# Performance work log

Measured on AMD Instinct MI355X. Metric: run time of the kernel, lower is better.

The kernel has to match this reference:

```python
import jax, jax.numpy as jnp
import numpy as np

N, E, D_IN, H, C, N_GRAPHS = 50000, 800000, 128, 2, 64, 50
D_HID = H * C  # 128
NEG_SLOPE = 0.2
EPS = 1e-16


def glorot(key, shape):
    fan_in, fan_out = shape[0], shape[-1]
    lim = jnp.sqrt(6.0 / (fan_in + fan_out))
    return jax.random.uniform(key, shape, jnp.float32, -lim, lim)


def setup_inputs() -> dict:
    key = jax.random.key(0)
    ks = jax.random.split(key, 12)
    x = jax.random.normal(ks[0], (N, D_IN), jnp.float32)
    edge_index = jax.random.randint(ks[1], (2, E), 0, N, jnp.int64)
    batch = jnp.sort(jax.random.randint(ks[2], (N,), 0, N_GRAPHS, jnp.int64))
    # GATConv layer 1: in=128 -> heads=2, out=64
    W1 = glorot(ks[3], (D_IN, H * C))
    as1 = glorot(ks[4], (1, H, C)).reshape(H, C)
    ad1 = glorot(ks[5], (1, H, C)).reshape(H, C)
    b1 = jnp.zeros((H * C,), jnp.float32)
    # GATConv layer 2: in=128 -> heads=2, out=64
    W2 = glorot(ks[6], (D_HID, H * C))
    as2 = glorot(ks[7], (1, H, C)).reshape(H, C)
    ad2 = glorot(ks[8], (1, H, C)).reshape(H, C)
    b2 = jnp.zeros((H * C,), jnp.float32)
    # Linear head: 128 -> 1
    Wh = glorot(ks[9], (D_HID, 1))
    bh = jnp.zeros((1,), jnp.float32)
    return {"x": x, "edge_index": edge_index, "batch": batch,
            "W1": W1, "as1": as1, "ad1": ad1, "b1": b1,
            "W2": W2, "as2": as2, "ad2": ad2, "b2": b2,
            "Wh": Wh, "bh": bh}


def gat_conv(x, src, dst, W, a_src, a_dst, bias):
    # PyG GATConv (concat=True, add_self_loops applied by caller, eval mode)
    n = x.shape[0]
    h = (x @ W).reshape(n, H, C)                       # [N,H,C]
    al_s = jnp.einsum('nhc,hc->nh', h, a_src)          # [N,H]
    al_d = jnp.einsum('nhc,hc->nh', h, a_dst)
    e = jax.nn.leaky_relu(al_s[src] + al_d[dst], NEG_SLOPE)  # [E',H]
    # segment softmax over incoming edges of each dst node
    e_max = jax.ops.segment_max(e, dst, num_segments=n)
    e = jnp.exp(e - e_max[dst])
    denom = jax.ops.segment_sum(e, dst, num_segments=n)
    alpha = e / (denom[dst] + EPS)                     # [E',H]
    out = jax.ops.segment_sum(alpha[:, :, None] * h[src], dst, num_segments=n)
    return out.reshape(n, H * C) + bias


def reference(x, edge_index, batch, W1, as1, ad1, b1, W2, as2, ad2, b2, Wh, bh):
    # add self-loops (PyG GATConv default)
    loops = jnp.arange(N, dtype=edge_index.dtype)
    src = jnp.concatenate([edge_index[0], loops])
    dst = jnp.concatenate([edge_index[1], loops])
    h = gat_conv(x, src, dst, W1, as1, ad1, b1)
    h = jax.nn.relu(h)  # dropout is identity in eval mode
    h = gat_conv(h, src, dst, W2, as2, ad2, b2)
    h = jax.nn.relu(h)
    # global mean pool over graphs
    sums = jax.ops.segment_sum(h, batch, num_segments=N_GRAPHS)
    counts = jax.ops.segment_sum(jnp.ones((N, 1), h.dtype), batch, num_segments=N_GRAPHS)
    pooled = sums / jnp.maximum(counts, 1.0)           # [G, 128]
    return pooled @ Wh + bh                            # [G, 1]
```

## Files before the change

### kernel.cpp

```cpp
#include <hip/hip_runtime.h>
#include <hip/hip_fp16.h>
#include <math.h>

#define HD 128
#define NEG_SLOPE 0.2f
#define EPSV 1e-16f
#define TILE 8192

typedef unsigned short ushort_t;
typedef __attribute__((ext_vector_type(8))) short bf16x8;
typedef __attribute__((ext_vector_type(4))) float f32x4;

__device__ inline void bsplit(float x, ushort_t& hi, ushort_t& lo) {
    unsigned u = __float_as_uint(x);
    unsigned hb = (u + 0x7FFFu + ((u >> 16) & 1u)) >> 16;
    hi = (ushort_t)hb;
    float res = x - __uint_as_float(hb << 16);
    unsigned v = __float_as_uint(res);
    lo = (ushort_t)((v + 0x7FFFu + ((v >> 16) & 1u)) >> 16);
}

__global__ __launch_bounds__(256) void part_hist(const int* __restrict__ dst,
                                                 int* __restrict__ tileHist, int E) {
    __shared__ int hist[256];
    int t = threadIdx.x;
    hist[t] = 0;
    __syncthreads();
    int base = blockIdx.x * TILE;
    int end = base + TILE; if (end > E) end = E;
    for (int i = base + t; i < end; i += 256)
        atomicAdd(&hist[dst[i] >> 8], 1);
    __syncthreads();
    tileHist[blockIdx.x * 256 + t] = hist[t];
}

__global__ __launch_bounds__(256) void part_offsets(int* __restrict__ tileHist,
                                                    int* __restrict__ bucketBase,
                                                    int NT) {
    __shared__ int s[256];
    int b = threadIdx.x;
    int total = 0;
    #pragma unroll 8
    for (int t = 0; t < NT; ++t) total += tileHist[t * 256 + b];
    s[b] = total;
    __syncthreads();
    for (int o = 1; o < 256; o <<= 1) {
        int v = (b >= o) ? s[b - o] : 0;
        __syncthreads();
        s[b] += v;
        __syncthreads();
    }
    int base = (b == 0) ? 0 : s[b - 1];
    bucketBase[b] = base;
    if (b == 255) bucketBase[256] = s[255];
    int run = base;
    #pragma unroll 8
    for (int t = 0; t < NT; ++t) {
        int v = tileHist[t * 256 + b];
        tileHist[t * 256 + b] = run;
        run += v;
    }
}

__global__ __launch_bounds__(256) void part_scatter(const int* __restrict__ src,
                                                    const int* __restrict__ dst,
                                                    const int* __restrict__ tileHist,
                                                    int* __restrict__ part, int E) {
    __shared__ int cur[256];
    int t = threadIdx.x;
    cur[t] = tileHist[blockIdx.x * 256 + t];
    __syncthreads();
    int base = blockIdx.x * TILE;
    int end = base + TILE; if (end > E) end = E;
    for (int i = base + t; i < end; i += 256) {
        int d = dst[i], s = src[i];
        int p = atomicAdd(&cur[d >> 8], 1);
        part[p] = (s << 8) | (d & 255);
    }
}

__global__ __launch_bounds__(256) void fine_counts(const int* __restrict__ part,
                                                   const int* __restrict__ bucketBase,
                                                   int* __restrict__ cnt,
                                                   int* __restrict__ bsum, int N) {
    __shared__ int hist[256];
    int t = threadIdx.x;
    hist[t] = 0;
    __syncthreads();
    int b = blockIdx.x;
    int s0 = bucketBase[b], s1 = bucketBase[b + 1];
    for (int i = s0 + t; i < s1; i += 256)
        atomicAdd(&hist[part[i] & 255], 1);
    __syncthreads();
    int d = b * 256 + t;
    if (d < N) cnt[d] = hist[t] + 1;
    if (t == 0) {
        int nn = N - b * 256; if (nn > 256) nn = 256; if (nn < 0) nn = 0;
        bsum[b] = (s1 - s0) + nn;
    }
}

__global__ __launch_bounds__(256) void scan_bsums(int* __restrict__ bsum, int NB) {
    __shared__ int s[256];
    __shared__ int carry;
    int t = threadIdx.x;
    if (t == 0) carry = 0;
    __syncthreads();
    for (int base = 0; base < NB; base += 256) {
        int i = base + t;
        int v = (i < NB) ? bsum[i] : 0;
        s[t] = v;
        __syncthreads();
        for (int o = 1; o < 256; o <<= 1) {
            int u = (t >= o) ? s[t - o] : 0;
            __syncthreads();
            s[t] += u;
            __syncthreads();
        }
        int excl = ((t == 0) ? 0 : s[t - 1]) + carry;
        if (i < NB) bsum[i] = excl;
        __syncthreads();
        if (t == 0) carry += s[255];
        __syncthreads();
    }
}

__global__ __launch_bounds__(256) void csr_scatter(const int* __restrict__ part,
                                                   const int* __restrict__ bucketBase,
                                                   const int* __restrict__ cnt,
                                                   const int* __restrict__ bsum,
                                                   int* __restrict__ indptr,
                                                   int* __restrict__ csr, int N) {
    __shared__ int s[256];
    __shared__ int cur[256];
    int t = threadIdx.x;
    int b = blockIdx.x;
    int d = b * 256 + t;
    int v = (d < N) ? cnt[d] : 0;
    s[t] = v;
    __syncthreads();
    for (int o = 1; o < 256; o <<= 1) {
        int u = (t >= o) ? s[t - o] : 0;
        __syncthreads();
        s[t] += u;
        __syncthreads();
    }
    int excl = ((t == 0) ? 0 : s[t - 1]) + bsum[b];
    if (d < N) indptr[d] = excl;
    if (d == N - 1) indptr[N] = excl + v;
    cur[t] = excl;
    __syncthreads();
    int s0 = bucketBase[b], s1 = bucketBase[b + 1];
    for (int i = s0 + t; i < s1; i += 256) {
        int e = part[i];
        int p = atomicAdd(&cur[e & 255], 1);
        csr[p] = e >> 8;
    }
    __syncthreads();
    if (d < N) csr[cur[t]] = d;
}

__global__ __launch_bounds__(256) void split_w(const float* __restrict__ W,
                                               ushort_t* __restrict__ Whs,
                                               ushort_t* __restrict__ Wls) {
    int idx = blockIdx.x * 256 + threadIdx.x;
    int j    = idx & 7;
    int lane = (idx >> 3) & 63;
    int ks   = (idx >> 9) & 3;
    int ct   = idx >> 11;
    int n = ct * 16 + (lane & 15);
    int k = ks * 32 + (lane >> 4) * 8 + j;
    ushort_t hi, lo;
    bsplit(W[k * 128 + n], hi, lo);
    Whs[idx] = hi;
    Wls[idx] = lo;
}

__device__ inline void load8(const float* p, float* vv) {
    float4 a = *(const float4*)p;
    float4 b = *(const float4*)(p + 4);
    vv[0]=a.x; vv[1]=a.y; vv[2]=a.z; vv[3]=a.w;
    vv[4]=b.x; vv[5]=b.y; vv[6]=b.z; vv[7]=b.w;
}
__device__ inline void load8(const __half* p, float* vv) {
    bf16x8 r = *(const bf16x8*)p;
    #pragma unroll
    for (int j = 0; j < 8; ++j)
        vv[j] = __half2float(__ushort_as_half((ushort_t)r[j]));
}

template <typename TA>
__global__ __launch_bounds__(256) void gemm_mfma(const TA* __restrict__ A,
                                                 const ushort_t* __restrict__ Whs,
                                                 const ushort_t* __restrict__ Wls,
                                                 const float* __restrict__ a_s,
                                                 const float* __restrict__ a_d,
                                                 __half* __restrict__ h16,
                                                 float* __restrict__ als,
                                                 float* __restrict__ ald, int N) {
    const int gw   = (blockIdx.x * 256 + threadIdx.x) >> 6;
    const int lane = threadIdx.x & 63;
    const int r0   = gw * 16;
    if (r0 >= N) return;
    const int m = lane & 15;
    const int q = lane >> 4;

    bf16x8 ah[4], al[4];
    {
        int row = r0 + m;
        if (row >= N) row = N - 1;
        const TA* ap = A + (size_t)row * HD;
        #pragma unroll
        for (int ks = 0; ks < 4; ++ks) {
            float vv[8];
            load8(ap + ks * 32 + q * 8, vv);
            #pragma unroll
            for (int j = 0; j < 8; ++j) {
                ushort_t hb, lb;
                bsplit(vv[j], hb, lb);
                ah[ks][j] = (short)hb;
                al[ks][j] = (short)lb;
            }
        }
    }

    float ps[4] = {0,0,0,0};
    float pd[4] = {0,0,0,0};

    #pragma unroll 1
    for (int ct = 0; ct < 8; ++ct) {
        f32x4 acc = {0.f, 0.f, 0.f, 0.f};
        #pragma unroll
        for (int ks = 0; ks < 4; ++ks) {
            bf16x8 wh = *(const bf16x8*)(Whs + ((size_t)(ct * 4 + ks) * 64 + lane) * 8);
            bf16x8 wl = *(const bf16x8*)(Wls + ((size_t)(ct * 4 + ks) * 64 + lane) * 8);
            acc = __builtin_amdgcn_mfma_f32_16x16x32_bf16(ah[ks], wh, acc, 0, 0, 0);
            acc = __builtin_amdgcn_mfma_f32_16x16x32_bf16(al[ks], wh, acc, 0, 0, 0);
            acc = __builtin_amdgcn_mfma_f32_16x16x32_bf16(ah[ks], wl, acc, 0, 0, 0);
        }
        const int col = ct * 16 + m;
        const float asv = a_s[col], adv = a_d[col];
        #pragma unroll
        for (int reg = 0; reg < 4; ++reg) {
            ps[reg] += acc[reg] * asv;
            pd[reg] += acc[reg] * adv;
            int row = r0 + q * 4 + reg;
            if (row < N) h16[(size_t)row * HD + col] = __float2half(acc[reg]);
        }
        if (ct == 3 || ct == 7) {
            int head = ct >> 2;
            #pragma unroll
            for (int reg = 0; reg < 4; ++reg) {
                float vs = ps[reg], vd = pd[reg];
                for (int o = 8; o >= 1; o >>= 1) {
                    vs += __shfl_xor(vs, o, 64);
                    vd += __shfl_xor(vd, o, 64);
                }
                if (m == 0) {
                    int row = r0 + q * 4 + reg;
                    if (row < N) { als[2 * row + head] = vs; ald[2 * row + head] = vd; }
                }
                ps[reg] = 0.f;  pd[reg] = 0.f;
            }
        }
    }
}

__global__ __launch_bounds__(256) void gat_aggregate(const __half* __restrict__ h,
                                                     const float* __restrict__ als,
                                                     const float* __restrict__ ald,
                                                     const int* __restrict__ indptr,
                                                     const int* __restrict__ csr,
                                                     const float* __restrict__ bias,
                                                     __half* __restrict__ out,
                                                     const float* __restrict__ Wh,
                                                     float* __restrict__ svec, int N) {
    __shared__ int2 ebuf[4][64];
    int w    = (blockIdx.x * blockDim.x + threadIdx.x) >> 6;
    int lane = threadIdx.x & 63;
    int wv   = (threadIdx.x >> 6);
    if (w >= N) return;
    int start = indptr[w], end = indptr[w + 1];
    float ad0 = ald[2 * w], ad1 = ald[2 * w + 1];
    const bool head0 = (lane < 32);
    const int cbase = lane * 2;

    float accx = 0.f, accy = 0.f, d0 = 0.f, d1 = 0.f;
    for (int base = start; base < end; base += 64) {
        int i = base + lane;
        int idx = i < end ? i : end - 1;
        int s = csr[idx];
        unsigned wpack = 0u;
        if (i < end) {
            float2 av = *(const float2*)&als[2 * s];
            float e0 = av.x + ad0;
            float e1 = av.y + ad1;
            e0 = e0 > 0.f ? e0 : NEG_SLOPE * e0;
            e1 = e1 > 0.f ? e1 : NEG_SLOPE * e1;
            __half p0 = __float2half(__expf(e0));
            __half p1 = __float2half(__expf(e1));
            wpack = ((unsigned)__half_as_ushort(p1) << 16) | __half_as_ushort(p0);
            d0 += __half2float(p0);
            d1 += __half2float(p1);
        }
        ebuf[wv][lane] = make_int2(s, (int)wpack);
        int nl = end - base; if (nl > 64) nl = 64;
        int nb = (nl + 7) >> 3;
        for (int b = 0; b < nb; ++b) {
            int j = b * 8;
            int2 e[8];
            #pragma unroll
            for (int u = 0; u < 8; ++u) e[u] = ebuf[wv][j + u];
            float wa[8];
            #pragma unroll
            for (int u = 0; u < 8; ++u) {
                unsigned wp = (unsigned)e[u].y;
                unsigned bits = head0 ? (wp & 0xffffu) : (wp >> 16);
                wa[u] = __half2float(__ushort_as_half((ushort_t)bits));
            }
            __half2 hv[8];
            #pragma unroll
            for (int u = 0; u < 8; ++u)
                hv[u] = *(const __half2*)&h[(size_t)e[u].x * HD + cbase];
            #pragma unroll
            for (int u = 0; u < 8; ++u) {
                float2 f = __half22float2(hv[u]);
                accx += wa[u] * f.x;
                accy += wa[u] * f.y;
            }
        }
    }
    for (int o = 32; o >= 1; o >>= 1) {
        d0 += __shfl_xor(d0, o, 64);
        d1 += __shfl_xor(d1, o, 64);
    }
    float D = (head0 ? d0 : d1) + EPSV;
    float ox = accx / D + bias[cbase];
    float oy = accy / D + bias[cbase + 1];
    ox = ox > 0.f ? ox : 0.f;
    oy = oy > 0.f ? oy : 0.f;

    if (svec) {
        float2 wv2 = *(const float2*)&Wh[cbase];
        float part = ox * wv2.x + oy * wv2.y;
        for (int o = 32; o >= 1; o >>= 1) part += __shfl_xor(part, o, 64);
        if (lane == 0) svec[w] = part;
    } else {
        *(__half2*)&out[(size_t)w * HD + cbase] =
            __halves2half2(__float2half(ox), __float2half(oy));
    }
}

__global__ void graph_bounds(const int* __restrict__ batch, int* __restrict__ gstart,
                             int N, int G) {
    int g = blockIdx.x * blockDim.x + threadIdx.x;
    if (g > G) return;
    int lo = 0, hi = N;
    while (lo < hi) {
        int mid = (lo + hi) >> 1;
        if (batch[mid] < g) lo = mid + 1; else hi = mid;
    }
    gstart[g] = lo;
}

__global__ __launch_bounds__(256) void pool_reduce(const float* __restrict__ s,
                                                   const int* __restrict__ gstart,
                                                   const float* __restrict__ bh,
                                                   float* __restrict__ out, int G) {
    __shared__ float partial[4];
    int g = blockIdx.x, t = threadIdx.x;
    int a = gstart[g], b = gstart[g + 1];
    float sum = 0.f;
    for (int i = a + t; i < b; i += 256) sum += s[i];
    for (int o = 32; o >= 1; o >>= 1) sum += __shfl_xor(sum, o, 64);
    if ((t & 63) == 0) partial[t >> 6] = sum;
    __syncthreads();
    if (t == 0) {
        float cnt = (float)(b - a); if (cnt < 1.f) cnt = 1.f;
        out[g] = (partial[0] + partial[1] + partial[2] + partial[3]) / cnt + bh[0];
    }
}

extern "C" void kernel_launch(void* const* d_in, const int* in_sizes, int n_in,
                              void* d_out, int out_size, void* d_ws, size_t ws_size,
                              hipStream_t stream) {
    const float* x     = (const float*)d_in[0];
    const int*   ei    = (const int*)d_in[1];
    const int*   batch = (const int*)d_in[2];
    const float* W1  = (const float*)d_in[3];
    const float* as1 = (const float*)d_in[4];
    const float* ad1 = (const float*)d_in[5];
    const float* b1  = (const float*)d_in[6];
    const float* W2  = (const float*)d_in[7];
    const float* as2 = (const float*)d_in[8];
    const float* ad2 = (const float*)d_in[9];
    const float* b2  = (const float*)d_in[10];
    const float* Wh  = (const float*)d_in[11];
    const float* bh  = (const float*)d_in[12];
    float* out = (float*)d_out;

    const int N = in_sizes[0] / HD;
    const int E = in_sizes[1] / 2;
    const int G = out_size;
    const int* srcp = ei;
    const int* dstp = ei + E;
    const int NBK = (N + 255) / 256;
    const int NT  = (E + TILE - 1) / TILE;

    char* ws = (char*)d_ws;
    size_t off = 0;
    auto alloc = [&](size_t bytes) -> void* {
        void* p = ws + off;
        off += (bytes + 255) & ~(size_t)255;
        return p;
    };
    __half* h16   = (__half*)alloc((size_t)N * HD * 2);
    __half* ob16  = (__half*)alloc((size_t)N * HD * 2);
    float* als    = (float*)alloc((size_t)N * 2 * 4);
    float* ald    = (float*)alloc((size_t)N * 2 * 4);
    float* svec   = (float*)alloc((size_t)N * 4);
    int*   indptr = (int*)  alloc((size_t)(N + 1) * 4);
    int*   cnt    = (int*)  alloc((size_t)N * 4);
    int*   bsum   = (int*)  alloc((size_t)NBK * 4);
    int*   csr    = (int*)  alloc((size_t)(E + N) * 4);
    int*   gstart = (int*)  alloc((size_t)(G + 1) * 4);
    int*   tileHist   = (int*)alloc((size_t)NT * 256 * 4);
    int*   bucketBase = (int*)alloc(257 * 4);
    int*   part   = (int*)  alloc((size_t)E * 4);
    ushort_t* Whs1 = (ushort_t*)alloc(16384 * 2);
    ushort_t* Wls1 = (ushort_t*)alloc(16384 * 2);
    ushort_t* Whs2 = (ushort_t*)alloc(16384 * 2);
    ushort_t* Wls2 = (ushort_t*)alloc(16384 * 2);

    part_hist<<<NT, 256, 0, stream>>>(dstp, tileHist, E);
    part_offsets<<<1, 256, 0, stream>>>(tileHist, bucketBase, NT);
    part_scatter<<<NT, 256, 0, stream>>>(srcp, dstp, tileHist, part, E);
    fine_counts<<<NBK, 256, 0, stream>>>(part, bucketBase, cnt, bsum, N);
    scan_bsums<<<1, 256, 0, stream>>>(bsum, NBK);
    csr_scatter<<<NBK, 256, 0, stream>>>(part, bucketBase, cnt, bsum, indptr, csr, N);
    graph_bounds<<<1, 64, 0, stream>>>(batch, gstart, N, G);

    split_w<<<64, 256, 0, stream>>>(W1, Whs1, Wls1);
    split_w<<<64, 256, 0, stream>>>(W2, Whs2, Wls2);

    const int nwaves  = (N + 15) / 16;
    const int gblocks = (nwaves + 3) / 4;
    int wgrid = (N * 64 + 255) / 256;

    gemm_mfma<<<gblocks, 256, 0, stream>>>(x, Whs1, Wls1, as1, ad1, h16, als, ald, N);
    gat_aggregate<<<wgrid, 256, 0, stream>>>(h16, als, ald, indptr, csr, b1, ob16,
                                             nullptr, nullptr, N);
    gemm_mfma<<<gblocks, 256, 0, stream>>>(ob16, Whs2, Wls2, as2, ad2, h16, als, ald, N);
    gat_aggregate<<<wgrid, 256, 0, stream>>>(h16, als, ald, indptr, csr, b2, nullptr,
                                             Wh, svec, N);
    pool_reduce<<<G, 256, 0, stream>>>(svec, gstart, bh, out, G);
}
```

Before: 254.5 us.

## Merge CSR build kernels, fuse weight splits, use fp16 MFMA for layer two

Replaces the fine_counts/scan_bsums/csr_scatter chain with one csr_build kernel. It computes indptr directly from the bucket base plus the local prefix and node index, which works because every node has exactly one self-loop. The two split_w launches become one, and the graph-bounds search moves into the pooling kernel. Layer two's GEMM now takes fp16 input directly and runs two fp16 MFMAs per k-step (A times W hi and lo) instead of three bf16 MFMAs with per-element splitting. The goal is fewer launches and less GEMM work, at the risk of slightly different precision in layer two.

Measured after the change: 247.2 us. -2.9%, faster.

```diff
diff --git a/kernel.cpp b/kernel.cpp
--- a/kernel.cpp
+++ b/kernel.cpp
@@ -9,6 +9,7 @@
 
 typedef unsigned short ushort_t;
 typedef __attribute__((ext_vector_type(8))) short bf16x8;
+typedef __attribute__((ext_vector_type(8))) _Float16 f16x8;
 typedef __attribute__((ext_vector_type(4))) float f32x4;
 
 __device__ inline void bsplit(float x, ushort_t& hi, ushort_t& lo) {
@@ -79,78 +80,36 @@
     }
 }
 
-__global__ __launch_bounds__(256) void fine_counts(const int* __restrict__ part,
-                                                   const int* __restrict__ bucketBase,
-                                                   int* __restrict__ cnt,
-                                                   int* __restrict__ bsum, int N) {
+__global__ __launch_bounds__(256) void csr_build(const int* __restrict__ part,
+                                                 const int* __restrict__ bucketBase,
+                                                 int* __restrict__ indptr,
+                                                 int* __restrict__ csr, int N, int E) {
     __shared__ int hist[256];
+    __shared__ int pfx[256];
+    __shared__ int cur[256];
     int t = threadIdx.x;
+    int b = blockIdx.x;
     hist[t] = 0;
     __syncthreads();
-    int b = blockIdx.x;
     int s0 = bucketBase[b], s1 = bucketBase[b + 1];
     for (int i = s0 + t; i < s1; i += 256)
         atomicAdd(&hist[part[i] & 255], 1);
     __syncthreads();
+    pfx[t] = hist[t];
+    __syncthreads();
+    for (int o = 1; o < 256; o <<= 1) {
+        int u = (t >= o) ? pfx[t - o] : 0;
+        __syncthreads();
+        pfx[t] += u;
+        __syncthreads();
+    }
+    int excl = (t == 0) ? 0 : pfx[t - 1];
     int d = b * 256 + t;
-    if (d < N) cnt[d] = hist[t] + 1;
-    if (t == 0) {
-        int nn = N - b * 256; if (nn > 256) nn = 256; if (nn < 0) nn = 0;
-        bsum[b] = (s1 - s0) + nn;
-    }
-}
-
-__global__ __launch_bounds__(256) void scan_bsums(int* __restrict__ bsum, int NB) {
-    __shared__ int s[256];
-    __shared__ int carry;
-    int t = threadIdx.x;
-    if (t == 0) carry = 0;
-    __syncthreads();
-    for (int base = 0; base < NB; base += 256) {
-        int i = base + t;
-        int v = (i < NB) ? bsum[i] : 0;
-        s[t] = v;
-        __syncthreads();
-        for (int o = 1; o < 256; o <<= 1) {
-            int u = (t >= o) ? s[t - o] : 0;
-            __syncthreads();
-            s[t] += u;
-            __syncthreads();
-        }
-        int excl = ((t == 0) ? 0 : s[t - 1]) + carry;
-        if (i < NB) bsum[i] = excl;
-        __syncthreads();
-        if (t == 0) carry += s[255];
-        __syncthreads();
-    }
-}
-
-__global__ __launch_bounds__(256) void csr_scatter(const int* __restrict__ part,
-                                                   const int* __restrict__ bucketBase,
-                                                   const int* __restrict__ cnt,
-                                                   const int* __restrict__ bsum,
-                                                   int* __restrict__ indptr,
-                                                   int* __restrict__ csr, int N) {
-    __shared__ int s[256];
-    __shared__ int cur[256];
-    int t = threadIdx.x;
-    int b = blockIdx.x;
-    int d = b * 256 + t;
-    int v = (d < N) ? cnt[d] : 0;
-    s[t] = v;
-    __syncthreads();
-    for (int o = 1; o < 256; o <<= 1) {
-        int u = (t >= o) ? s[t - o] : 0;
-        __syncthreads();
-        s[t] += u;
-        __syncthreads();
-    }
-    int excl = ((t == 0) ? 0 : s[t - 1]) + bsum[b];
-    if (d < N) indptr[d] = excl;
-    if (d == N - 1) indptr[N] = excl + v;
-    cur[t] = excl;
-    __syncthreads();
-    int s0 = bucketBase[b], s1 = bucketBase[b + 1];
+    int ip = s0 + excl + d;
+    if (d < N) indptr[d] = ip;
+    if (b == 0 && t == 0) indptr[N] = E + N;
+    cur[t] = ip;
+    __syncthreads();
     for (int i = s0 + t; i < s1; i += 256) {
         int e = part[i];
         int p = atomicAdd(&cur[e & 255], 1);
@@ -160,37 +119,36 @@
     if (d < N) csr[cur[t]] = d;
 }
 
-__global__ __launch_bounds__(256) void split_w(const float* __restrict__ W,
-                                               ushort_t* __restrict__ Whs,
-                                               ushort_t* __restrict__ Wls) {
-    int idx = blockIdx.x * 256 + threadIdx.x;
+__global__ __launch_bounds__(256) void split_w(const float* __restrict__ W1,
+                                               const float* __restrict__ W2,
+                                               ushort_t* __restrict__ Whs1,
+                                               ushort_t* __restrict__ Wls1,
+                                               ushort_t* __restrict__ Whs2,
+                                               ushort_t* __restrict__ Wls2) {
+    int blk = blockIdx.x & 63;
+    bool layer2 = blockIdx.x >= 64;
+    int idx = blk * 256 + threadIdx.x;
     int j    = idx & 7;
     int lane = (idx >> 3) & 63;
     int ks   = (idx >> 9) & 3;
     int ct   = idx >> 11;
     int n = ct * 16 + (lane & 15);
     int k = ks * 32 + (lane >> 4) * 8 + j;
-    ushort_t hi, lo;
-    bsplit(W[k * 128 + n], hi, lo);
-    Whs[idx] = hi;
-    Wls[idx] = lo;
-}
-
-__device__ inline void load8(const float* p, float* vv) {
-    float4 a = *(const float4*)p;
-    float4 b = *(const float4*)(p + 4);
-    vv[0]=a.x; vv[1]=a.y; vv[2]=a.z; vv[3]=a.w;
-    vv[4]=b.x; vv[5]=b.y; vv[6]=b.z; vv[7]=b.w;
-}
-__device__ inline void load8(const __half* p, float* vv) {
-    bf16x8 r = *(const bf16x8*)p;
-    #pragma unroll
-    for (int j = 0; j < 8; ++j)
-        vv[j] = __half2float(__ushort_as_half((ushort_t)r[j]));
-}
-
-template <typename TA>
-__global__ __launch_bounds__(256) void gemm_mfma(const TA* __restrict__ A,
+    if (!layer2) {
+        ushort_t hi, lo;
+        bsplit(W1[k * 128 + n], hi, lo);
+        Whs1[idx] = hi;
+        Wls1[idx] = lo;
+    } else {
+        float v = W2[k * 128 + n];
+        __half h = __float2half(v);
+        __half l = __float2half(v - __half2float(h));
+        Whs2[idx] = __half_as_ushort(h);
+        Wls2[idx] = __half_as_ushort(l);
+    }
+}
+
+__global__ __launch_bounds__(256) void gemm_mfma(const float* __restrict__ A,
                                                  const ushort_t* __restrict__ Whs,
                                                  const ushort_t* __restrict__ Wls,
                                                  const float* __restrict__ a_s,
@@ -209,11 +167,12 @@
     {
         int row = r0 + m;
         if (row >= N) row = N - 1;
-        const TA* ap = A + (size_t)row * HD;
+        const float* ap = A + (size_t)row * HD;
         #pragma unroll
         for (int ks = 0; ks < 4; ++ks) {
-            float vv[8];
-            load8(ap + ks * 32 + q * 8, vv);
+            float4 v0 = *(const float4*)(ap + ks * 32 + q * 8);
+            float4 v1 = *(const float4*)(ap + ks * 32 + q * 8 + 4);
+            float vv[8] = {v0.x, v0.y, v0.z, v0.w, v1.x, v1.y, v1.z, v1.w};
             #pragma unroll
             for (int j = 0; j < 8; ++j) {
                 ushort_t hb, lb;
@@ -237,6 +196,72 @@
             acc = __builtin_amdgcn_mfma_f32_16x16x32_bf16(ah[ks], wh, acc, 0, 0, 0);
             acc = __builtin_amdgcn_mfma_f32_16x16x32_bf16(al[ks], wh, acc, 0, 0, 0);
             acc = __builtin_amdgcn_mfma_f32_16x16x32_bf16(ah[ks], wl, acc, 0, 0, 0);
+        }
+        const int col = ct * 16 + m;
+        const float asv = a_s[col], adv = a_d[col];
+        #pragma unroll
+        for (int reg = 0; reg < 4; ++reg) {
+            ps[reg] += acc[reg] * asv;
+            pd[reg] += acc[reg] * adv;
+            int row = r0 + q * 4 + reg;
+            if (row < N) h16[(size_t)row * HD + col] = __float2half(acc[reg]);
+        }
+        if (ct == 3 || ct == 7) {
+            int head = ct >> 2;
+            #pragma unroll
+            for (int reg = 0; reg < 4; ++reg) {
+                float vs = ps[reg], vd = pd[reg];
+                for (int o = 8; o >= 1; o >>= 1) {
+                    vs += __shfl_xor(vs, o, 64);
+                    vd += __shfl_xor(vd, o, 64);
+                }
+                if (m == 0) {
+                    int row = r0 + q * 4 + reg;
+                    if (row < N) { als[2 * row + head] = vs; ald[2 * row + head] = vd; }
+                }
+                ps[reg] = 0.f;  pd[reg] = 0.f;
+            }
+        }
+    }
+}
+
+__global__ __launch_bounds__(256) void gemm_mfma_f16(const __half* __restrict__ A,
+                                                     const ushort_t* __restrict__ Whs,
+                                                     const ushort_t* __restrict__ Wls,
+                                                     const float* __restrict__ a_s,
+                                                     const float* __restrict__ a_d,
+                                                     __half* __restrict__ h16,
+                                                     float* __restrict__ als,
+                                                     float* __restrict__ ald, int N) {
+    const int gw   = (blockIdx.x * 256 + threadIdx.x) >> 6;
+    const int lane = threadIdx.x & 63;
+    const int r0   = gw * 16;
+    if (r0 >= N) return;
+    const int m = lane & 15;
+    const int q = lane >> 4;
+
+    f16x8 ah[4];
+    {
+        int row = r0 + m;
+        if (row >= N) row = N - 1;
+        const __half* ap = A + (size_t)row * HD;
+        #pragma unroll
+        for (int ks = 0; ks < 4; ++ks)
+            ah[ks] = *(const f16x8*)(ap + ks * 32 + q * 8);
+    }
+
+    float ps[4] = {0,0,0,0};
+    float pd[4] = {0,0,0,0};
+
+    #pragma unroll 1
+    for (int ct = 0; ct < 8; ++ct) {
+        f32x4 acc = {0.f, 0.f, 0.f, 0.f};
+        #pragma unroll
+        for (int ks = 0; ks < 4; ++ks) {
+            f16x8 wh = *(const f16x8*)(Whs + ((size_t)(ct * 4 + ks) * 64 + lane) * 8);
+            f16x8 wl = *(const f16x8*)(Wls + ((size_t)(ct * 4 + ks) * 64 + lane) * 8);
+            acc = __builtin_amdgcn_mfma_f32_16x16x32_f16(ah[ks], wh, acc, 0, 0, 0);
+            acc = __builtin_amdgcn_mfma_f32_16x16x32_f16(ah[ks], wl, acc, 0, 0, 0);
         }
         const int col = ct * 16 + m;
         const float asv = a_s[col], adv = a_d[col];
@@ -351,25 +376,21 @@
     }
 }
 
-__global__ void graph_bounds(const int* __restrict__ batch, int* __restrict__ gstart,
-                             int N, int G) {
-    int g = blockIdx.x * blockDim.x + threadIdx.x;
-    if (g > G) return;
-    int lo = 0, hi = N;
-    while (lo < hi) {
-        int mid = (lo + hi) >> 1;
-        if (batch[mid] < g) lo = mid + 1; else hi = mid;
-    }
-    gstart[g] = lo;
-}
-
-__global__ __launch_bounds__(256) void pool_reduce(const float* __restrict__ s,
-                                                   const int* __restrict__ gstart,
-                                                   const float* __restrict__ bh,
-                                                   float* __restrict__ out, int G) {
+__global__ __launch_bounds__(256) void pool_head(const float* __restrict__ s,
+                                                 const int* __restrict__ batch,
+                                                 const float* __restrict__ bh,
+                                                 float* __restrict__ out, int N, int G) {
     __shared__ float partial[4];
     int g = blockIdx.x, t = threadIdx.x;
-    int a = gstart[g], b = gstart[g + 1];
+    auto lb = [&](int key) {
+        int lo = 0, hi = N;
+        while (lo < hi) {
+            int mid = (lo + hi) >> 1;
+            if (batch[mid] < key) lo = mid + 1; else hi = mid;
+        }
+        return lo;
+    };
+    int a = lb(g), b = lb(g + 1);
     float sum = 0.f;
     for (int i = a + t; i < b; i += 256) sum += s[i];
     for (int o = 32; o >= 1; o >>= 1) sum += __shfl_xor(sum, o, 64);
@@ -420,10 +441,7 @@
     float* ald    = (float*)alloc((size_t)N * 2 * 4);
     float* svec   = (float*)alloc((size_t)N * 4);
     int*   indptr = (int*)  alloc((size_t)(N + 1) * 4);
-    int*   cnt    = (int*)  alloc((size_t)N * 4);
-    int*   bsum   = (int*)  alloc((size_t)NBK * 4);
     int*   csr    = (int*)  alloc((size_t)(E + N) * 4);
-    int*   gstart = (int*)  alloc((size_t)(G + 1) * 4);
     int*   tileHist   = (int*)alloc((size_t)NT * 256 * 4);
     int*   bucketBase = (int*)alloc(257 * 4);
     int*   part   = (int*)  alloc((size_t)E * 4);
@@ -435,13 +453,9 @@
     part_hist<<<NT, 256, 0, stream>>>(dstp, tileHist, E);
     part_offsets<<<1, 256, 0, stream>>>(tileHist, bucketBase, NT);
     part_scatter<<<NT, 256, 0, stream>>>(srcp, dstp, tileHist, part, E);
-    fine_counts<<<NBK, 256, 0, stream>>>(part, bucketBase, cnt, bsum, N);
-    scan_bsums<<<1, 256, 0, stream>>>(bsum, NBK);
-    csr_scatter<<<NBK, 256, 0, stream>>>(part, bucketBase, cnt, bsum, indptr, csr, N);
-    graph_bounds<<<1, 64, 0, stream>>>(batch, gstart, N, G);
-
-    split_w<<<64, 256, 0, stream>>>(W1, Whs1, Wls1);
-    split_w<<<64, 256, 0, stream>>>(W2, Whs2, Wls2);
+    csr_build<<<NBK, 256, 0, stream>>>(part, bucketBase, indptr, csr, N, E);
+
+    split_w<<<128, 256, 0, stream>>>(W1, W2, Whs1, Wls1, Whs2, Wls2);
 
     const int nwaves  = (N + 15) / 16;
     const int gblocks = (nwaves + 3) / 4;
@@ -450,8 +464,9 @@
     gemm_mfma<<<gblocks, 256, 0, stream>>>(x, Whs1, Wls1, as1, ad1, h16, als, ald, N);
     gat_aggregate<<<wgrid, 256, 0, stream>>>(h16, als, ald, indptr, csr, b1, ob16,
                                              nullptr, nullptr, N);
-    gemm_mfma<<<gblocks, 256, 0, stream>>>(ob16, Whs2, Wls2, as2, ad2, h16, als, ald, N);
+    gemm_mfma_f16<<<gblocks, 256, 0, stream>>>(ob16, Whs2, Wls2, as2, ad2, h16,
+                                               als, ald, N);
     gat_aggregate<<<wgrid, 256, 0, stream>>>(h16, als, ald, indptr, csr, b2, nullptr,
                                              Wh, svec, N);
-    pool_reduce<<<G, 256, 0, stream>>>(svec, gstart, bh, out, G);
-}
+    pool_head<<<G, 256, 0, stream>>>(svec, batch, bh, out, N, G);
+}
```
